# Performance work log

Hardware: AMD Instinct MI355X
Metric: run time of the kernel (lower is better)

## Reference

```python
import jax, jax.numpy as jnp
import numpy as np

B, I, L = 128, 32, 96   # batch, input_dim, time_series_length
H = 512                  # hidden_dim
F = 24                   # forecast_length (t_eval points)
S = 16                   # n_samples


def _lin(k, out_dim, in_dim):
    kw, kb = jax.random.split(k)
    bound = 1.0 / np.sqrt(in_dim)
    W = jax.random.uniform(kw, (out_dim, in_dim), jnp.float32, -bound, bound)
    b = jax.random.uniform(kb, (out_dim,), jnp.float32, -bound, bound)
    return W, b


def setup_inputs() -> dict:
    key = jax.random.key(0)
    ks = jax.random.split(key, 12)
    enc_Wih, enc_bih = _lin(ks[0], 3 * H, I)
    enc_Whh, enc_bhh = _lin(ks[1], 3 * H, H)
    f_W1, f_b1 = _lin(ks[2], H, H)
    f_W2, f_b2 = _lin(ks[3], H, H)
    g_W, g_b = _lin(ks[4], H, H)
    dec_Wih, dec_bih = _lin(ks[5], 3 * H, H)
    dec_Whh, dec_bhh = _lin(ks[6], 3 * H, H)
    out_W, out_b = _lin(ks[7], I, H)
    x = jax.random.normal(ks[8], (B, I, L), jnp.float32)
    noise = jax.random.normal(ks[9], (S, F - 1, B, H), jnp.float32)  # unit normals -> dW = sqrt(dt)*noise
    return dict(x=x, noise=noise,
                enc_Wih=enc_Wih, enc_Whh=enc_Whh, enc_bih=enc_bih, enc_bhh=enc_bhh,
                f_W1=f_W1, f_b1=f_b1, f_W2=f_W2, f_b2=f_b2,
                g_W=g_W, g_b=g_b,
                dec_Wih=dec_Wih, dec_Whh=dec_Whh, dec_bih=dec_bih, dec_bhh=dec_bhh,
                out_W=out_W, out_b=out_b)


def _gru_cell(gi, gh, h):
    ir, iz, inn = jnp.split(gi, 3, axis=-1)
    hr, hz, hn = jnp.split(gh, 3, axis=-1)
    r = jax.nn.sigmoid(ir + hr)
    z = jax.nn.sigmoid(iz + hz)
    n = jnp.tanh(inn + r * hn)
    return (1.0 - z) * n + z * h


def reference(x, noise, enc_Wih, enc_Whh, enc_bih, enc_bhh,
              f_W1, f_b1, f_W2, f_b2, g_W, g_b,
              dec_Wih, dec_Whh, dec_bih, dec_bhh, out_W, out_b):
    Bb, Ii = x.shape[0], x.shape[1]
    Ss, steps = noise.shape[0], noise.shape[1]
    Hh = enc_Whh.shape[1]
    Ff = steps + 1  # forecast_length; t_eval=linspace(0,F,F) -> F-1 euler steps

    # ---- encoder GRU over [B, L, I] (x permuted from [B, I, L]) ----
    xs = jnp.transpose(x, (0, 2, 1))  # [B, L, I]
    gi_all = jnp.einsum('bli,gi->lbg', xs, enc_Wih) + enc_bih  # [L, B, 3H]

    def enc_step(h, gi):
        gh = h @ enc_Whh.T + enc_bhh
        return _gru_cell(gi, gh, h), None

    h0 = jnp.zeros((Bb, Hh), x.dtype)
    h_enc, _ = jax.lax.scan(enc_step, h0, gi_all)  # [B, H]

    # ---- Euler-Maruyama SDE integration, samples merged into batch ----
    dt = Ff / steps  # linspace(0, F, F): dt = F/(F-1)
    sqdt = jnp.sqrt(jnp.asarray(dt, x.dtype))
    h_sde = jnp.broadcast_to(h_enc, (Ss, Bb, Hh)).reshape(Ss * Bb, Hh)
    dW = (noise * sqdt).transpose(1, 0, 2, 3).reshape(steps, Ss * Bb, Hh)

    def sde_step(h, dw):
        f = jnp.tanh(h @ f_W1.T + f_b1) @ f_W2.T + f_b2
        g = jax.nn.softplus(h @ g_W.T + g_b)
        return h + f * dt + g * dw, None

    h_T, _ = jax.lax.scan(sde_step, h_sde, dW)  # [S*B, H]

    # ---- decoder GRU with zero inputs (input proj reduces to bias) ----
    gi0 = dec_bih  # W_ih @ 0 + b_ih

    def dec_step(h, _):
        gh = h @ dec_Whh.T + dec_bhh
        h_new = _gru_cell(gi0, gh, h)
        return h_new, h_new

    _, hs = jax.lax.scan(dec_step, h_T, None, length=Ff)  # [F, S*B, H]

    out = hs @ out_W.T + out_b          # [F, S*B, I]
    out = out.transpose(1, 2, 0)        # [S*B, I, F]
    return out.reshape(Ss, Bb, Ii, Ff)  # [S, B, I, F]
```

## Files before the change

kernel.cpp:

```cpp
#include <hip/hip_runtime.h>
#include <math.h>

typedef __bf16 bf16x8 __attribute__((ext_vector_type(8)));
typedef float f32x4 __attribute__((ext_vector_type(4)));
typedef unsigned int u32x4 __attribute__((ext_vector_type(4)));
typedef unsigned long long u64;

#define HD 512
#define NB 128
#define NI 32
#define NL 96
#define NS 16
#define NF 24
#define NSTEP 23
#define PAD 520

#define MFMA16(a,b,c) __builtin_amdgcn_mfma_f32_16x16x32_bf16(a,b,c,0,0,0)

__device__ __forceinline__ unsigned short f2bf(float f) {
    union { float f; unsigned u; } v; v.f = f;
    unsigned r = v.u + 0x7fffu + ((v.u >> 16) & 1u);
    return (unsigned short)(r >> 16);
}
__device__ __forceinline__ float bf2f(unsigned short h) {
    union { unsigned u; float f; } v; v.u = ((unsigned)h) << 16;
    return v.f;
}
__device__ __forceinline__ void split_bf(float v, unsigned short& hi, unsigned short& lo) {
    unsigned short h = f2bf(v);
    hi = h;
    lo = f2bf(v - bf2f(h));
}
__device__ __forceinline__ float sigm(float x) { return 1.0f / (1.0f + __expf(-x)); }
__device__ __forceinline__ float softp(float x) {
    return fmaxf(x, 0.0f) + log1pf(__expf(-fabsf(x)));
}
__device__ __forceinline__ bf16x8 ld8(const unsigned short* p) {
    return *reinterpret_cast<const bf16x8*>(p);
}
__device__ __forceinline__ f32x4 mfma3(bf16x8 ahi, bf16x8 alo, const unsigned short* bp, f32x4 c) {
    bf16x8 bhi = ld8(bp);
    bf16x8 blo = ld8(bp + 8);
    c = MFMA16(ahi, bhi, c);
    c = MFMA16(alo, bhi, c);
    c = MFMA16(ahi, blo, c);
    return c;
}

__device__ __forceinline__ void ld16i(const void* p, u32x4& d) {
    asm volatile("global_load_dwordx4 %0, %1, off sc0 sc1"
                 : "=&v"(d) : "v"(p) : "memory");
}
__device__ __forceinline__ void ldfence() {
    asm volatile("s_waitcnt vmcnt(0)" ::: "memory");
    __builtin_amdgcn_sched_barrier(0);
}

__device__ __forceinline__ void sigval(unsigned* slot, unsigned val, int tid) {
    __builtin_amdgcn_s_waitcnt(0);
    __syncthreads();
    if (tid == 0)
        __hip_atomic_store(slot, val, __ATOMIC_RELAXED, __HIP_MEMORY_SCOPE_AGENT);
}
__device__ __forceinline__ void poll4(const unsigned* f, unsigned tgt, int wv, int lane) {
    if (wv == 0) {
        for (;;) {
            unsigned v = __hip_atomic_load(f + (lane & 3), __ATOMIC_RELAXED, __HIP_MEMORY_SCOPE_AGENT);
            if (__all((int)(v >= tgt))) break;
            __builtin_amdgcn_s_sleep(2);
        }
    }
    __syncthreads();
}
__device__ __forceinline__ void stage32(const u64* sh, const u64* sl, int r0,
        unsigned short (*Ahi)[16][PAD], unsigned short (*Alo)[16][PAD], int tid) {
    u32x4 th[4], tl[4];
    #pragma unroll
    for (int k = 0; k < 4; ++k) {
        int idx = k * 512 + tid;
        int r = idx >> 6, c8 = idx & 63;
        ld16i(sh + (size_t)(r0 + r) * 128 + c8 * 2, th[k]);
        ld16i(sl + (size_t)(r0 + r) * 128 + c8 * 2, tl[k]);
    }
    ldfence();
    #pragma unroll
    for (int k = 0; k < 4; ++k) {
        int idx = k * 512 + tid;
        int r = idx >> 6, c8 = idx & 63;
        *(u32x4*)&Ahi[r >> 4][r & 15][c8 * 8] = th[k];
        *(u32x4*)&Alo[r >> 4][r & 15][c8 * 8] = tl[k];
    }
}
__device__ __forceinline__ void publish32(u64* dh, u64* dl, int r0, int u0c,
        unsigned short (*Bhi)[136], unsigned short (*Blo)[136], int tid) {
    #pragma unroll
    for (int rep = 0; rep < 4; ++rep) {
        int idx = rep * 512 + tid;
        int pl = idx >> 10, e = idx & 1023;
        int r = e >> 5, c = e & 31;
        u64 q = pl ? *(const u64*)&Blo[r][c * 4] : *(const u64*)&Bhi[r][c * 4];
        u64* dst = (pl ? dl : dh) + (size_t)(r0 + r) * 128 + u0c + c;
        __hip_atomic_store(dst, q, __ATOMIC_RELAXED, __HIP_MEMORY_SCOPE_AGENT);
    }
}

__global__ void pack_w(const float* __restrict__ W, unsigned short* __restrict__ Wp,
                       int N, int K) {
    int idx = blockIdx.x * 256 + threadIdx.x;
    int total = (N / 16) * (K / 32) * 64;
    if (idx >= total) return;
    int lane = idx & 63;
    int t2 = idx >> 6;
    int KT = K / 32;
    int kt = t2 % KT, nt = t2 / KT;
    const float* src = W + (size_t)(nt * 16 + (lane & 15)) * K + kt * 32 + (lane >> 4) * 8;
    unsigned short* dst = Wp + (size_t)idx * 16;
    #pragma unroll
    for (int j = 0; j < 8; ++j) split_bf(src[j], dst[j], dst[8 + j]);
}

__global__ void pack_x(const float* __restrict__ x, unsigned short* __restrict__ xhi,
                       unsigned short* __restrict__ xlo) {
    int idx = blockIdx.x * 256 + threadIdx.x;
    if (idx >= NL * NB) return;
    int b = idx % NB, l = idx / NB;
    size_t base = (size_t)(l * NB + b) * NI;
    #pragma unroll
    for (int i = 0; i < NI; ++i)
        split_bf(x[((size_t)b * NI + i) * NL + l], xhi[base + i], xlo[base + i]);
}

__global__ __launch_bounds__(512, 2) void coop_all(
    const unsigned short* __restrict__ xhi, const unsigned short* __restrict__ xlo,
    const unsigned short* __restrict__ wih_p, const unsigned short* __restrict__ whh_p,
    const unsigned short* __restrict__ w1_p, const unsigned short* __restrict__ w2_p,
    const unsigned short* __restrict__ gw_p, const unsigned short* __restrict__ dwhh_p,
    const unsigned short* __restrict__ outw_p,
    const float* __restrict__ ebih, const float* __restrict__ ebhh,
    const float* __restrict__ fb1, const float* __restrict__ fb2,
    const float* __restrict__ gb, const float* __restrict__ dbih,
    const float* __restrict__ dbhh, const float* __restrict__ outb,
    const float* __restrict__ noise,
    u64* hS0h, u64* hS0l, u64* hS1h, u64* hS1l,
    u64* uPh, u64* uPl, u64* hD0h, u64* hD0l, u64* hD1h, u64* hD1l,
    float* out, unsigned* bar)
{
    const int bid = blockIdx.x;
    const int tid = threadIdx.x, lane = tid & 63, wv = tid >> 6;
    const int l15 = lane & 15, g4 = lane >> 4;
    const f32x4 zz = {0.f, 0.f, 0.f, 0.f};

    __shared__ __align__(16) unsigned char SM[83968];
    auto hA32hi = reinterpret_cast<unsigned short (*)[16][PAD]>(SM);
    auto hA32lo = reinterpret_cast<unsigned short (*)[16][PAD]>(SM + 33280);
    auto uShi   = reinterpret_cast<unsigned short (*)[136]>(SM + 66560);
    auto uSlo   = reinterpret_cast<unsigned short (*)[136]>(SM + 75264);
    auto pred   = reinterpret_cast<float (*)[8][16][16]>(SM);
    auto ehAhi  = reinterpret_cast<unsigned short (*)[PAD]>(SM + 32768);
    auto ehAlo  = reinterpret_cast<unsigned short (*)[PAD]>(SM + 49408);
    auto Shi    = reinterpret_cast<unsigned short (*)[16]>(SM + 66048);
    auto Slo    = reinterpret_cast<unsigned short (*)[16]>(SM + 66560);

    u64* bufh[2] = {hS0h, hS1h};
    u64* bufl[2] = {hS0l, hS1l};

    {
        const int m = bid >> 5, n = bid & 31;
        unsigned* fl = bar + m * 32;
        float cr = 0.f, cz = 0.f, binx = 0.f, bhnn = 0.f, hcell = 0.f;
        const int crow = tid >> 4, cunit = tid & 15;
        if (tid < 256) {
            int u = n * 16 + cunit;
            cr = ebih[u] + ebhh[u];
            cz = ebih[HD + u] + ebhh[HD + u];
            binx = ebih[2 * HD + u];
            bhnn = ebhh[2 * HD + u];
        }
        #pragma unroll 1
        for (int l = 0; l < NL; ++l) {
            bf16x8 axh, axl;
            if (wv == 0) {
                size_t xb = ((size_t)l * NB + m * 16 + l15) * NI + g4 * 8;
                axh = ld8(xhi + xb);
                axl = ld8(xlo + xb);
            }
            if (l > 0) {
                if (wv == 0) {
                    for (;;) {
                        unsigned v = __hip_atomic_load(fl + (lane & 31),
                                     __ATOMIC_RELAXED, __HIP_MEMORY_SCOPE_AGENT);
                        if (__all((int)(v >= (unsigned)l))) break;
                        __builtin_amdgcn_s_sleep(2);
                    }
                }
                __syncthreads();
            }
            {
                const u64* sh = bufh[l & 1];
                const u64* sl = bufl[l & 1];
                u32x4 qh[2], ql[2];
                #pragma unroll
                for (int rep = 0; rep < 2; ++rep) {
                    int idx = rep * 512 + tid;
                    int r = idx >> 6, c8 = idx & 63;
                    ld16i(sh + (size_t)(m * 16 + r) * 128 + c8 * 2, qh[rep]);
                    ld16i(sl + (size_t)(m * 16 + r) * 128 + c8 * 2, ql[rep]);
                }
                ldfence();
                #pragma unroll
                for (int rep = 0; rep < 2; ++rep) {
                    int idx = rep * 512 + tid;
                    int r = idx >> 6, c8 = idx & 63;
                    *(u32x4*)&ehAhi[r][c8 * 8] = qh[rep];
                    *(u32x4*)&ehAlo[r][c8 * 8] = ql[rep];
                }
            }
            __syncthreads();
            f32x4 pr = zz, pz = zz, pnh = zz, pnx = zz;
            if (wv == 0) {
                pr  = mfma3(axh, axl, wih_p + ((size_t)(0 * 32 + n) * 64 + lane) * 16, pr);
                pz  = mfma3(axh, axl, wih_p + ((size_t)(1 * 32 + n) * 64 + lane) * 16, pz);
                pnx = mfma3(axh, axl, wih_p + ((size_t)(2 * 32 + n) * 64 + lane) * 16, pnx);
            }
            #pragma unroll
            for (int kk = 0; kk < 2; ++kk) {
                int kt = wv * 2 + kk;
                bf16x8 ah = *(const bf16x8*)&ehAhi[l15][kt * 32 + g4 * 8];
                bf16x8 al = *(const bf16x8*)&ehAlo[l15][kt * 32 + g4 * 8];
                pr  = mfma3(ah, al, whh_p + ((size_t)((0 * 32 + n) * 16 + kt) * 64 + lane) * 16, pr);
                pz  = mfma3(ah, al, whh_p + ((size_t)((1 * 32 + n) * 16 + kt) * 64 + lane) * 16, pz);
                pnh = mfma3(ah, al, whh_p + ((size_t)((2 * 32 + n) * 16 + kt) * 64 + lane) * 16, pnh);
            }
            #pragma unroll
            for (int v = 0; v < 4; ++v) {
                pred[0][wv][g4 * 4 + v][l15] = pr[v];
                pred[1][wv][g4 * 4 + v][l15] = pz[v];
                pred[2][wv][g4 * 4 + v][l15] = pnh[v];
                if (wv == 0) pred[3][0][g4 * 4 + v][l15] = pnx[v];
            }
            __syncthreads();
            if (tid < 256) {
                float ar = 0.f, az = 0.f, anh_ = 0.f;
                #pragma unroll
                for (int w = 0; w < 8; ++w) {
                    ar += pred[0][w][crow][cunit];
                    az += pred[1][w][crow][cunit];
                    anh_ += pred[2][w][crow][cunit];
                }
                float anx_ = pred[3][0][crow][cunit];
                float r = sigm(ar + cr);
                float z = sigm(az + cz);
                float nn = tanhf(anx_ + binx + r * (anh_ + bhnn));
                hcell = (1.f - z) * nn + z * hcell;
                unsigned short hi, lo;
                split_bf(hcell, hi, lo);
                Shi[crow][cunit] = hi;
                Slo[crow][cunit] = lo;
            }
            __syncthreads();
            if (tid < 128) {
                int p = tid >> 6, t = tid & 63;
                int r = t >> 2, c4 = t & 3;
                u64 q = p ? *(const u64*)&Slo[r][c4 * 4] : *(const u64*)&Shi[r][c4 * 4];
                u64* dst = p ? bufl[(l + 1) & 1] : bufh[(l + 1) & 1];
                __hip_atomic_store(dst + (size_t)(m * 16 + r) * 128 + n * 4 + c4, q,
                                   __ATOMIC_RELAXED, __HIP_MEMORY_SCOPE_AGENT);
            }
            __builtin_amdgcn_s_waitcnt(0);
            __syncthreads();
            if (tid == 0)
                __hip_atomic_store(fl + n, (unsigned)(l + 1),
                                   __ATOMIC_RELAXED, __HIP_MEMORY_SCOPE_AGENT);
        }
        if (tid == 0)
            __hip_atomic_fetch_add(bar + 256, 1u, __ATOMIC_RELAXED, __HIP_MEMORY_SCOPE_AGENT);
    }

    if (tid == 0) {
        while (__hip_atomic_load(bar + 256, __ATOMIC_RELAXED, __HIP_MEMORY_SCOPE_AGENT) < 256u)
            __builtin_amdgcn_s_sleep(2);
    }
    __syncthreads();

    const int m2 = bid >> 2, n2 = bid & 3;
    const int rt = wv & 1, nc = wv >> 1;
    const int r0g = m2 * 32;
    const int u0 = n2 * 128, u0c = n2 * 32;
    const int s = m2 >> 2, b0 = (m2 & 3) * 32;
    unsigned* uf = bar + 320 + m2 * 4;
    unsigned* hf = bar + 576 + m2 * 4;
    u64* hDh[2] = {hD0h, hD1h};
    u64* hDl[2] = {hD0l, hD1l};

    stage32(hS0h, hS0l, b0, hA32hi, hA32lo, tid);
    __syncthreads();

    float hreg[2][4];
    #pragma unroll
    for (int nt = 0; nt < 2; ++nt)
        #pragma unroll
        for (int v = 0; v < 4; ++v) {
            int cc = u0 + nc * 32 + nt * 16 + l15;
            hreg[nt][v] = bf2f(hA32hi[rt][g4 * 4 + v][cc]) + bf2f(hA32lo[rt][g4 * 4 + v][cc]);
        }

    float b1v[2], b2v[2], gbv[2];
    #pragma unroll
    for (int nt = 0; nt < 2; ++nt) {
        int u = u0 + nc * 32 + nt * 16 + l15;
        b1v[nt] = fb1[u]; b2v[nt] = fb2[u]; gbv[nt] = gb[u];
    }
    const float dt = (float)NF / (float)NSTEP;
    const float sqdt = sqrtf(dt);

    #pragma unroll 1
    for (int st = 0; st < NSTEP; ++st) {
        f32x4 au[2] = {zz, zz}, ag[2] = {zz, zz};
        #pragma unroll 2
        for (int kt = 0; kt < 16; ++kt) {
            bf16x8 ah = *(const bf16x8*)&hA32hi[rt][l15][kt * 32 + g4 * 8];
            bf16x8 al = *(const bf16x8*)&hA32lo[rt][l15][kt * 32 + g4 * 8];
            #pragma unroll
            for (int nt = 0; nt < 2; ++nt) {
                int ntg = n2 * 8 + nc * 2 + nt;
                au[nt] = mfma3(ah, al, w1_p + ((size_t)(ntg * 16 + kt) * 64 + lane) * 16, au[nt]);
                ag[nt] = mfma3(ah, al, gw_p + ((size_t)(ntg * 16 + kt) * 64 + lane) * 16, ag[nt]);
            }
        }
        float nz[2][4];
        #pragma unroll
        for (int nt = 0; nt < 2; ++nt)
            #pragma unroll
            for (int v = 0; v < 4; ++v)
                nz[nt][v] = noise[((size_t)(s * NSTEP + st) * NB + b0 + rt * 16 + g4 * 4 + v) * HD
                                  + u0 + nc * 32 + nt * 16 + l15];
        #pragma unroll
        for (int nt = 0; nt < 2; ++nt)
            #pragma unroll
            for (int v = 0; v < 4; ++v) {
                unsigned short hi, lo;
                split_bf(tanhf(au[nt][v] + b1v[nt]), hi, lo);
                uShi[rt * 16 + g4 * 4 + v][nc * 32 + nt * 16 + l15] = hi;
                uSlo[rt * 16 + g4 * 4 + v][nc * 32 + nt * 16 + l15] = lo;
            }
        __syncthreads();
        publish32(uPh, uPl, r0g, u0c, uShi, uSlo, tid);
        sigval(uf + n2, (unsigned)(st + 1), tid);
        poll4(uf, (unsigned)(st + 1), wv, lane);
        stage32(uPh, uPl, r0g, hA32hi, hA32lo, tid);
        __syncthreads();
        f32x4 af[2] = {zz, zz};
        #pragma unroll 2
        for (int kt = 0; kt < 16; ++kt) {
            bf16x8 uh = *(const bf16x8*)&hA32hi[rt][l15][kt * 32 + g4 * 8];
            bf16x8 ul = *(const bf16x8*)&hA32lo[rt][l15][kt * 32 + g4 * 8];
            #pragma unroll
            for (int nt = 0; nt < 2; ++nt) {
                int ntg = n2 * 8 + nc * 2 + nt;
                af[nt] = mfma3(uh, ul, w2_p + ((size_t)(ntg * 16 + kt) * 64 + lane) * 16, af[nt]);
            }
        }
        #pragma unroll
        for (int nt = 0; nt < 2; ++nt)
            #pragma unroll
            for (int v = 0; v < 4; ++v) {
                float gg = softp(ag[nt][v] + gbv[nt]);
                hreg[nt][v] += (af[nt][v] + b2v[nt]) * dt + gg * sqdt * nz[nt][v];
                unsigned short hi, lo;
                split_bf(hreg[nt][v], hi, lo);
                uShi[rt * 16 + g4 * 4 + v][nc * 32 + nt * 16 + l15] = hi;
                uSlo[rt * 16 + g4 * 4 + v][nc * 32 + nt * 16 + l15] = lo;
            }
        __syncthreads();
        publish32(hDh[(st + 1) & 1], hDl[(st + 1) & 1], r0g, u0c, uShi, uSlo, tid);
        sigval(hf + n2, (unsigned)(st + 1), tid);
        poll4(hf, (unsigned)(st + 1), wv, lane);
        stage32(hDh[(st + 1) & 1], hDl[(st + 1) & 1], r0g, hA32hi, hA32lo, tid);
        __syncthreads();
    }

    float crv[2], czv[2], binv[2], bhnv[2];
    #pragma unroll
    for (int nt = 0; nt < 2; ++nt) {
        int u = u0 + nc * 32 + nt * 16 + l15;
        crv[nt] = dbih[u] + dbhh[u];
        czv[nt] = dbih[HD + u] + dbhh[HD + u];
        binv[nt] = dbih[2 * HD + u];
        bhnv[nt] = dbhh[2 * HD + u];
    }
    float obias[2] = {0.f, 0.f};
    if (n2 == 0 && nc == 0) {
        obias[0] = outb[l15];
        obias[1] = outb[16 + l15];
    }

    #pragma unroll 1
    for (int j = 0; j <= NF; ++j) {
        if (j >= 1 && n2 == 0 && nc == 0) {
            f32x4 ao[2] = {zz, zz};
            #pragma unroll 2
            for (int kt = 0; kt < 16; ++kt) {
                bf16x8 ah = *(const bf16x8*)&hA32hi[rt][l15][kt * 32 + g4 * 8];
                bf16x8 al = *(const bf16x8*)&hA32lo[rt][l15][kt * 32 + g4 * 8];
                #pragma unroll
                for (int nt = 0; nt < 2; ++nt)
                    ao[nt] = mfma3(ah, al, outw_p + ((size_t)(nt * 16 + kt) * 64 + lane) * 16, ao[nt]);
            }
            #pragma unroll
            for (int nt = 0; nt < 2; ++nt)
                #pragma unroll
                for (int v = 0; v < 4; ++v) {
                    int b = b0 + rt * 16 + g4 * 4 + v;
                    out[(((size_t)s * NB + b) * NI + nt * 16 + l15) * NF + (j - 1)]
                        = ao[nt][v] + obias[nt];
                }
        }
        if (j == NF) break;
        f32x4 ar[2] = {zz, zz}, az[2] = {zz, zz}, anh[2] = {zz, zz};
        #pragma unroll 2
        for (int kt = 0; kt < 16; ++kt) {
            bf16x8 ah = *(const bf16x8*)&hA32hi[rt][l15][kt * 32 + g4 * 8];
            bf16x8 al = *(const bf16x8*)&hA32lo[rt][l15][kt * 32 + g4 * 8];
            #pragma unroll
            for (int nt = 0; nt < 2; ++nt) {
                int ntg = n2 * 8 + nc * 2 + nt;
                ar[nt]  = mfma3(ah, al, dwhh_p + ((size_t)((ntg) * 16 + kt) * 64 + lane) * 16, ar[nt]);
                az[nt]  = mfma3(ah, al, dwhh_p + ((size_t)((32 + ntg) * 16 + kt) * 64 + lane) * 16, az[nt]);
                anh[nt] = mfma3(ah, al, dwhh_p + ((size_t)((64 + ntg) * 16 + kt) * 64 + lane) * 16, anh[nt]);
            }
        }
        #pragma unroll
        for (int nt = 0; nt < 2; ++nt)
            #pragma unroll
            for (int v = 0; v < 4; ++v) {
                float r = sigm(ar[nt][v] + crv[nt]);
                float z = sigm(az[nt][v] + czv[nt]);
                float nn2 = tanhf(binv[nt] + r * (anh[nt][v] + bhnv[nt]));
                hreg[nt][v] = (1.f - z) * nn2 + z * hreg[nt][v];
                unsigned short hi, lo;
                split_bf(hreg[nt][v], hi, lo);
                uShi[rt * 16 + g4 * 4 + v][nc * 32 + nt * 16 + l15] = hi;
                uSlo[rt * 16 + g4 * 4 + v][nc * 32 + nt * 16 + l15] = lo;
            }
        __syncthreads();
        publish32(hDh[(NSTEP + j + 1) & 1], hDl[(NSTEP + j + 1) & 1], r0g, u0c, uShi, uSlo, tid);
        sigval(hf + n2, (unsigned)(NSTEP + j + 1), tid);
        poll4(hf, (unsigned)(NSTEP + j + 1), wv, lane);
        stage32(hDh[(NSTEP + j + 1) & 1], hDl[(NSTEP + j + 1) & 1], r0g, hA32hi, hA32lo, tid);
        __syncthreads();
    }
}

extern "C" void kernel_launch(void* const* d_in, const int* in_sizes, int n_in,
                              void* d_out, int out_size, void* d_ws, size_t ws_size,
                              hipStream_t stream) {
    const float* x       = (const float*)d_in[0];
    const float* noise   = (const float*)d_in[1];
    const float* enc_Wih = (const float*)d_in[2];
    const float* enc_Whh = (const float*)d_in[3];
    const float* enc_bih = (const float*)d_in[4];
    const float* enc_bhh = (const float*)d_in[5];
    const float* f_W1    = (const float*)d_in[6];
    const float* f_b1    = (const float*)d_in[7];
    const float* f_W2    = (const float*)d_in[8];
    const float* f_b2    = (const float*)d_in[9];
    const float* g_W     = (const float*)d_in[10];
    const float* g_b     = (const float*)d_in[11];
    const float* dec_Whh = (const float*)d_in[13];
    const float* dec_bih = (const float*)d_in[14];
    const float* dec_bhh = (const float*)d_in[15];
    const float* out_W   = (const float*)d_in[16];
    const float* out_b   = (const float*)d_in[17];
    float* out = (float*)d_out;

    char* ws = (char*)d_ws;
    unsigned short* whh_p  = (unsigned short*)(ws + 0);
    unsigned short* wih_p  = (unsigned short*)(ws + 3145728);
    unsigned short* w1_p   = (unsigned short*)(ws + 3342336);
    unsigned short* w2_p   = (unsigned short*)(ws + 4390912);
    unsigned short* gw_p   = (unsigned short*)(ws + 5439488);
    unsigned short* dwhh_p = (unsigned short*)(ws + 6488064);
    unsigned short* outw_p = (unsigned short*)(ws + 9633792);
    unsigned short* xhi    = (unsigned short*)(ws + 9699328);
    unsigned short* xlo    = (unsigned short*)(ws + 10485760);
    u64*            hS0h   = (u64*)(ws + 11272192);
    u64*            hS0l   = (u64*)(ws + 11403264);
    u64*            hS1h   = (u64*)(ws + 11534336);
    u64*            hS1l   = (u64*)(ws + 11665408);
    unsigned*       bar    = (unsigned*)(ws + 11796480);
    u64*            uPh    = (u64*)(ws + 11800576);
    u64*            uPl    = (u64*)(ws + 13897728);
    u64*            hD0h   = (u64*)(ws + 15994880);
    u64*            hD0l   = (u64*)(ws + 18092032);
    u64*            hD1h   = (u64*)(ws + 20189184);
    u64*            hD1l   = (u64*)(ws + 22286336);

    hipMemsetAsync(ws + 11272192, 0, 262144, stream);
    hipMemsetAsync(ws + 11796480, 0, 4096, stream);

    pack_w<<<384, 256, 0, stream>>>(enc_Whh, whh_p, 3 * HD, HD);
    pack_w<<<24, 256, 0, stream>>>(enc_Wih, wih_p, 3 * HD, NI);
    pack_w<<<128, 256, 0, stream>>>(f_W1, w1_p, HD, HD);
    pack_w<<<128, 256, 0, stream>>>(f_W2, w2_p, HD, HD);
    pack_w<<<128, 256, 0, stream>>>(g_W, gw_p, HD, HD);
    pack_w<<<384, 256, 0, stream>>>(dec_Whh, dwhh_p, 3 * HD, HD);
    pack_w<<<8, 256, 0, stream>>>(out_W, outw_p, NI, HD);
    pack_x<<<48, 256, 0, stream>>>(x, xhi, xlo);

    void* args[] = {
        (void*)&xhi, (void*)&xlo, (void*)&wih_p, (void*)&whh_p,
        (void*)&w1_p, (void*)&w2_p, (void*)&gw_p, (void*)&dwhh_p, (void*)&outw_p,
        (void*)&enc_bih, (void*)&enc_bhh, (void*)&f_b1, (void*)&f_b2,
        (void*)&g_b, (void*)&dec_bih, (void*)&dec_bhh, (void*)&out_b,
        (void*)&noise,
        (void*)&hS0h, (void*)&hS0l, (void*)&hS1h, (void*)&hS1l,
        (void*)&uPh, (void*)&uPl, (void*)&hD0h, (void*)&hD0l, (void*)&hD1h, (void*)&hD1l,
        (void*)&out, (void*)&bar
    };
    hipLaunchCooperativeKernel((void*)coop_all, dim3(256), dim3(512), args, 0, stream);
}
```

Baseline: 1.715 ms.

## Stage only peer slices from global and overlap own-slice MFMA with barrier wait

In the SDE and decoder loops each block now copies its own 128-column slice of the shared hidden/u state straight from LDS instead of re-reading it from global memory after the grid barrier. Only the three peer blocks' slices are staged from global. In the f-net second matmul, the MFMA work for the block's own K-slice is issued before polling the barrier flag, so computation overlaps the wait. The poll sleep interval is also shortened. Together these aim to cut global traffic and latency on the critical cross-block synchronisation path, at the cost of more complex indexing and a dependence on the own-slice column layout matching u0.

```diff
diff --git a/kernel.cpp b/kernel.cpp
--- a/kernel.cpp
+++ b/kernel.cpp
@@ -67,7 +67,7 @@
         for (;;) {
             unsigned v = __hip_atomic_load(f + (lane & 3), __ATOMIC_RELAXED, __HIP_MEMORY_SCOPE_AGENT);
             if (__all((int)(v >= tgt))) break;
-            __builtin_amdgcn_s_sleep(2);
+            __builtin_amdgcn_s_sleep(1);
         }
     }
     __syncthreads();
@@ -89,6 +89,48 @@
         int r = idx >> 6, c8 = idx & 63;
         *(u32x4*)&Ahi[r >> 4][r & 15][c8 * 8] = th[k];
         *(u32x4*)&Alo[r >> 4][r & 15][c8 * 8] = tl[k];
+    }
+}
+__device__ __forceinline__ void stage_peers(const u64* sh, const u64* sl, int r0, int n2,
+        unsigned short (*Ahi)[16][PAD], unsigned short (*Alo)[16][PAD], int tid) {
+    u32x4 t[6];
+    #pragma unroll
+    for (int k = 0; k < 6; ++k) {
+        int it = k * 512 + tid;
+        int pl = (it >= 1536) ? 1 : 0;
+        int e = it - pl * 1536;
+        int p = e >> 9;
+        int w = e & 511;
+        int r = w >> 4, c16 = w & 15;
+        int q = (n2 + 1 + p) & 3;
+        const u64* src = (pl ? sl : sh) + (size_t)(r0 + r) * 128 + q * 32 + c16 * 2;
+        ld16i(src, t[k]);
+    }
+    ldfence();
+    #pragma unroll
+    for (int k = 0; k < 6; ++k) {
+        int it = k * 512 + tid;
+        int pl = (it >= 1536) ? 1 : 0;
+        int e = it - pl * 1536;
+        int p = e >> 9;
+        int w = e & 511;
+        int r = w >> 4, c16 = w & 15;
+        int q = (n2 + 1 + p) & 3;
+        unsigned short (*A)[16][PAD] = pl ? Alo : Ahi;
+        *(u32x4*)&A[r >> 4][r & 15][q * 128 + c16 * 8] = t[k];
+    }
+}
+__device__ __forceinline__ void own_copy(unsigned short (*Shi_)[136], unsigned short (*Slo_)[136],
+        int u0s, unsigned short (*Ahi)[16][PAD], unsigned short (*Alo)[16][PAD], int tid) {
+    #pragma unroll
+    for (int k = 0; k < 2; ++k) {
+        int it = k * 512 + tid;
+        int pl = (it >= 512) ? 1 : 0;
+        int w = it & 511;
+        int r = w >> 4, c16 = w & 15;
+        u32x4 v = pl ? *(const u32x4*)&Slo_[r][c16 * 8] : *(const u32x4*)&Shi_[r][c16 * 8];
+        unsigned short (*A)[16][PAD] = pl ? Alo : Ahi;
+        *(u32x4*)&A[r >> 4][r & 15][u0s + c16 * 8] = v;
     }
 }
 __device__ __forceinline__ void publish32(u64* dh, u64* dl, int r0, int u0c,
@@ -190,7 +232,7 @@
                         unsigned v = __hip_atomic_load(fl + (lane & 31),
                                      __ATOMIC_RELAXED, __HIP_MEMORY_SCOPE_AGENT);
                         if (__all((int)(v >= (unsigned)l))) break;
-                        __builtin_amdgcn_s_sleep(2);
+                        __builtin_amdgcn_s_sleep(1);
                     }
                 }
                 __syncthreads();
@@ -346,12 +388,24 @@
         __syncthreads();
         publish32(uPh, uPl, r0g, u0c, uShi, uSlo, tid);
         sigval(uf + n2, (unsigned)(st + 1), tid);
+        f32x4 af[2] = {zz, zz};
+        #pragma unroll
+        for (int kk = 0; kk < 4; ++kk) {
+            int kt = n2 * 4 + kk;
+            bf16x8 uh = *(const bf16x8*)&uShi[rt * 16 + l15][kk * 32 + g4 * 8];
+            bf16x8 ul = *(const bf16x8*)&uSlo[rt * 16 + l15][kk * 32 + g4 * 8];
+            #pragma unroll
+            for (int nt = 0; nt < 2; ++nt) {
+                int ntg = n2 * 8 + nc * 2 + nt;
+                af[nt] = mfma3(uh, ul, w2_p + ((size_t)(ntg * 16 + kt) * 64 + lane) * 16, af[nt]);
+            }
+        }
         poll4(uf, (unsigned)(st + 1), wv, lane);
-        stage32(uPh, uPl, r0g, hA32hi, hA32lo, tid);
+        stage_peers(uPh, uPl, r0g, n2, hA32hi, hA32lo, tid);
         __syncthreads();
-        f32x4 af[2] = {zz, zz};
         #pragma unroll 2
         for (int kt = 0; kt < 16; ++kt) {
+            if ((kt >> 2) == n2) continue;
             bf16x8 uh = *(const bf16x8*)&hA32hi[rt][l15][kt * 32 + g4 * 8];
             bf16x8 ul = *(const bf16x8*)&hA32lo[rt][l15][kt * 32 + g4 * 8];
             #pragma unroll
@@ -374,8 +428,9 @@
         __syncthreads();
         publish32(hDh[(st + 1) & 1], hDl[(st + 1) & 1], r0g, u0c, uShi, uSlo, tid);
         sigval(hf + n2, (unsigned)(st + 1), tid);
+        own_copy(uShi, uSlo, u0, hA32hi, hA32lo, tid);
         poll4(hf, (unsigned)(st + 1), wv, lane);
-        stage32(hDh[(st + 1) & 1], hDl[(st + 1) & 1], r0g, hA32hi, hA32lo, tid);
+        stage_peers(hDh[(st + 1) & 1], hDl[(st + 1) & 1], r0g, n2, hA32hi, hA32lo, tid);
         __syncthreads();
     }
 
@@ -445,8 +500,9 @@
         __syncthreads();
         publish32(hDh[(NSTEP + j + 1) & 1], hDl[(NSTEP + j + 1) & 1], r0g, u0c, uShi, uSlo, tid);
         sigval(hf + n2, (unsigned)(NSTEP + j + 1), tid);
+        own_copy(uShi, uSlo, u0, hA32hi, hA32lo, tid);
         poll4(hf, (unsigned)(NSTEP + j + 1), wv, lane);
-        stage32(hDh[(NSTEP + j + 1) & 1], hDl[(NSTEP + j + 1) & 1], r0g, hA32hi, hA32lo, tid);
+        stage_peers(hDh[(NSTEP + j + 1) & 1], hDl[(NSTEP + j + 1) & 1], r0g, n2, hA32hi, hA32lo, tid);
         __syncthreads();
     }
 }
```

After: 1.696 ms. Within noise of the previous version (-1.1%).
